# Optimization experiments

Measured on AMD Instinct MI355X. Metric: run time of the kernel, lower is better.

## Reference

```python
import jax, jax.numpy as jnp
import numpy as np

B, S, DIN, DOUT = 4, 4096, 2048, 8192


def setup_inputs() -> dict:
    key = jax.random.key(0)
    k1, k2 = jax.random.split(key)
    x = jax.random.normal(k1, (B, S, DIN), dtype=jnp.float32)
    # kaiming_normal_ (fan_in mode, leaky_relu a=sqrt(5) default -> gain based) approx via std = sqrt(2/fan_in)
    weight = jax.random.normal(k2, (DOUT, DIN), dtype=jnp.float32) * np.sqrt(2.0 / DIN)
    bias = jnp.zeros((DOUT,), dtype=jnp.float32)
    gamma = jnp.ones((DIN,), dtype=jnp.float32)
    return {"x": x, "weight": weight, "bias": bias, "gamma": gamma}


def reference(x, weight, bias, gamma):
    # RMSNorm in fp32 (torch nn.RMSNorm, eps=None -> finfo(fp32).eps)
    eps = jnp.asarray(np.finfo(np.float32).eps, dtype=jnp.float32)
    ms = jnp.mean(x * x, axis=-1, keepdims=True)  # [B,S,1]
    xn = x * jax.lax.rsqrt(ms + eps) * gamma      # [B,S,DIN]
    # Ternary quantize weights: threshold = mean(|w|), values in {-1,0,+1}; STE for grads
    thr = jnp.mean(jnp.abs(weight))
    w_t = jnp.sign(weight) * (jnp.abs(weight) > thr).astype(weight.dtype)
    w = weight + jax.lax.stop_gradient(w_t - weight)
    # Linear: out = xn @ w.T + bias
    out = jnp.einsum('bsi,oi->bso', xn, w) + bias
    return out
```

## Files before the change

kernel.cpp:

```cpp
#include <hip/hip_runtime.h>

typedef unsigned short u16;
typedef unsigned int   u32;
typedef unsigned char  u8;
typedef __attribute__((ext_vector_type(4))) int   i32x4;

constexpr int B_ = 4, S_ = 4096, DIN_ = 2048, DOUT_ = 8192;
constexpr int M_ = B_ * S_;
constexpr int N_ = DOUT_;
constexpr int K_ = DIN_;
constexpr size_t NW_ = (size_t)DOUT_ * DIN_;

#define GPTR(p) ((const __attribute__((address_space(1))) void*)(p))
#define LPTR(p) ((__attribute__((address_space(3))) void*)(p))

#define SB0()   __builtin_amdgcn_sched_barrier(0)
#define BAR()   asm volatile("s_barrier" ::: "memory")
#define LGKM0() asm volatile("s_waitcnt lgkmcnt(0)" ::: "memory")
#define VM4()   asm volatile("s_waitcnt vmcnt(4)" ::: "memory")
#define VM0()   asm volatile("s_waitcnt vmcnt(0)" ::: "memory")

__global__ __launch_bounds__(256)
void abssum_kernel(const float* __restrict__ w, double* __restrict__ partials)
{
    const int tid = threadIdx.x;
    const float* base = w + (size_t)blockIdx.x * 16384 + tid * 4;
    double s = 0.0;
#pragma unroll
    for (int i = 0; i < 16; ++i) {
        float4 v = *(const float4*)(base + i * 1024);
        s += (double)fabsf(v.x) + (double)fabsf(v.y)
           + (double)fabsf(v.z) + (double)fabsf(v.w);
    }
#pragma unroll
    for (int o = 32; o; o >>= 1) s += __shfl_xor(s, o, 64);
    __shared__ double red[4];
    if ((tid & 63) == 0) red[tid >> 6] = s;
    __syncthreads();
    if (tid == 0) partials[blockIdx.x] = (red[0] + red[1]) + (red[2] + red[3]);
}

__global__ __launch_bounds__(1024)
void finalize_thr(const double* __restrict__ partials, double* __restrict__ thr)
{
    __shared__ double red[1024];
    const int tid = threadIdx.x;
    red[tid] = partials[tid];
    __syncthreads();
    for (int s = 512; s > 0; s >>= 1) {
        if (tid < s) red[tid] += red[tid + s];
        __syncthreads();
    }
    if (tid == 0) *thr = red[0] * (1.0 / (double)NW_);
}

__device__ __forceinline__ int tern(float w, double thr) {
    return (fabs((double)w) > thr) ? (w > 0.0f ? 1 : -1) : 0;
}

__global__ __launch_bounds__(256)
void ternarize_kernel(const float* __restrict__ w, const double* __restrict__ thr_p,
                      signed char* __restrict__ wt)
{
    const double thr = *thr_p;
    const size_t i = ((size_t)blockIdx.x * 256 + threadIdx.x) * 4;
    float4 v = *(const float4*)(w + i);
    union { signed char c[4]; u32 u; } p;
    p.c[0] = (signed char)tern(v.x, thr);
    p.c[1] = (signed char)tern(v.y, thr);
    p.c[2] = (signed char)tern(v.z, thr);
    p.c[3] = (signed char)tern(v.w, thr);
    *(u32*)(wt + i) = p.u;
}

__global__ __launch_bounds__(256)
void rmsnorm_q_kernel(const float* __restrict__ x, const float* __restrict__ gamma,
                      signed char* __restrict__ xn, float* __restrict__ scale)
{
    const int row = blockIdx.x;
    const int tid = threadIdx.x;
    const float* xr = x + (size_t)row * K_;
    float4 a = *(const float4*)(xr + tid * 8);
    float4 b = *(const float4*)(xr + tid * 8 + 4);
    float s = a.x*a.x + a.y*a.y + a.z*a.z + a.w*a.w
            + b.x*b.x + b.y*b.y + b.z*b.z + b.w*b.w;
#pragma unroll
    for (int o = 32; o; o >>= 1) s += __shfl_xor(s, o, 64);
    __shared__ float redsum[4];
    __shared__ float redmax[4];
    if ((tid & 63) == 0) redsum[tid >> 6] = s;
    __syncthreads();
    const float tot = (redsum[0] + redsum[1]) + (redsum[2] + redsum[3]);
    const float r = rsqrtf(tot * (1.0f / (float)K_) + 1.1920928955078125e-07f);
    float4 g0 = *(const float4*)(gamma + tid * 8);
    float4 g1 = *(const float4*)(gamma + tid * 8 + 4);
    float v[8];
    v[0] = a.x * r * g0.x;  v[1] = a.y * r * g0.y;
    v[2] = a.z * r * g0.z;  v[3] = a.w * r * g0.w;
    v[4] = b.x * r * g1.x;  v[5] = b.y * r * g1.y;
    v[6] = b.z * r * g1.z;  v[7] = b.w * r * g1.w;
    float m = 0.0f;
#pragma unroll
    for (int j = 0; j < 8; ++j) m = fmaxf(m, fabsf(v[j]));
#pragma unroll
    for (int o = 32; o; o >>= 1) m = fmaxf(m, __shfl_xor(m, o, 64));
    if ((tid & 63) == 0) redmax[tid >> 6] = m;
    __syncthreads();
    const float rowmax = fmaxf(fmaxf(redmax[0], redmax[1]), fmaxf(redmax[2], redmax[3]));
    const float inv = rowmax > 0.0f ? 127.0f / rowmax : 0.0f;
    union { signed char c[8]; uint2 u; } p;
#pragma unroll
    for (int j = 0; j < 8; ++j) p.c[j] = (signed char)__float2int_rn(v[j] * inv);
    *(uint2*)(xn + (size_t)row * K_ + tid * 8) = p.u;
    if (tid == 0) scale[row] = rowmax * (1.0f / 127.0f);
}

__global__ __launch_bounds__(512, 2)
void gemm_bt_kernel(const u8* __restrict__ A, const u8* __restrict__ Bt,
                    const float* __restrict__ bias, const float* __restrict__ scale,
                    float* __restrict__ C)
{
    __shared__ alignas(16) u8 sm[131072];
    const char* smc = (const char*)sm;

    const int tid  = threadIdx.x;
    const int lane = tid & 63;
    const int wid  = tid >> 6;
    const int wm   = wid >> 2;
    const int wn   = wid & 3;
    const int hi   = lane >> 4;

    const int swz = (blockIdx.x & 7) * 256 + (blockIdx.x >> 3);
    const int gm0 = (swz >> 5) * 256;
    const int gn0 = (swz & 31) * 256;

    const int lr8   = lane >> 3;
    const int cswel = ((lane & 7) ^ lr8) * 16;
    const int rbase = wid * 8 + lr8;
    const u8* gAr  = A  + (size_t)(gm0 + rbase) * K_ + cswel;
    const u8* gBr  = Bt + (size_t)(gn0 + rbase) * K_ + cswel;
    const u8* gAr2 = gAr + 262144;
    const u8* gBr2 = gBr + 262144;

    auto STAGE = [&](const u8* g, int ldsb, int kt) {
        u8* d = sm + ldsb + wid * 1024 + lane * 16;
        const u8* s = g + kt;
        __builtin_amdgcn_global_load_lds(GPTR(s),             LPTR(d),        16, 0, 0);
        __builtin_amdgcn_global_load_lds(GPTR(s + 64 * 2048), LPTR(d + 8192), 16, 0, 0);
    };

    const int c0 = ((hi ^ (lane & 7)) << 4);
    const int rowbyteA = (wm * 128 + (lane & 15)) * 128;
    const int rowbyteB = (wn * 64  + (lane & 15)) * 128;

#define RA(bufr, m, kk) (*(const i32x4*)(smc + (bufr)*32768 + rowbyteA + (m)*2048 + (c0 ^ ((kk) << 6))))
#define RB(bufr, n, kk) (*(const i32x4*)(smc + 65536 + (bufr)*32768 + rowbyteB + (n)*2048 + (c0 ^ ((kk) << 6))))

    i32x4 acc[8][4] = {};
    i32x4 a0[4][2], a1[4][2], b0[2][2], b1[2][2];

#define MFMA_BLK(AF, BF, MO, NO)                                                   \
    do {                                                                           \
        _Pragma("unroll") for (int kk = 0; kk < 2; ++kk)                           \
        _Pragma("unroll") for (int m = 0; m < 4; ++m)                              \
        _Pragma("unroll") for (int n = 0; n < 2; ++n)                              \
            acc[m + MO][n + NO] = __builtin_amdgcn_mfma_i32_16x16x64_i8(           \
                AF[m][kk], BF[n][kk], acc[m + MO][n + NO], 0, 0, 0);               \
    } while (0)

#define READ_A0B0(bufr)                                                            \
    do {                                                                           \
        _Pragma("unroll") for (int m = 0; m < 4; ++m) {                            \
            a0[m][0] = RA(bufr, m, 0); a0[m][1] = RA(bufr, m, 1); }                \
        _Pragma("unroll") for (int n = 0; n < 2; ++n) {                            \
            b0[n][0] = RB(bufr, n, 0); b0[n][1] = RB(bufr, n, 1); }                \
    } while (0)
#define READ_A1(bufr)                                                              \
    do { _Pragma("unroll") for (int m = 0; m < 4; ++m) {                           \
            a1[m][0] = RA(bufr, m + 4, 0); a1[m][1] = RA(bufr, m + 4, 1); } } while (0)
#define READ_B1(bufr)                                                              \
    do { _Pragma("unroll") for (int n = 0; n < 2; ++n) {                           \
            b1[n][0] = RB(bufr, n + 2, 0); b1[n][1] = RB(bufr, n + 2, 1); } } while (0)

#define PRIO_MFMA(AF, BF, MO, NO)                                                  \
    do { __builtin_amdgcn_s_setprio(1); MFMA_BLK(AF, BF, MO, NO);                  \
         __builtin_amdgcn_s_setprio(0); } while (0)

    STAGE(gAr,  0,     0);
    STAGE(gAr2, 16384, 0);
    STAGE(gBr,  65536, 0);
    STAGE(gBr2, 81920, 0);
    STAGE(gAr,  32768, 128);
    STAGE(gAr2, 49152, 128);
    VM4(); SB0(); BAR();

    for (int i = 0; i < 8; ++i) {
        const int kt1  = i * 256 + 128;
        const int ktn0 = i * 256 + 256;
        const int ktn1 = i * 256 + 384;
        const bool f = (i < 7);

        READ_A0B0(0);
        STAGE(gBr, 98304, kt1);
        SB0(); BAR(); LGKM0(); SB0();
        PRIO_MFMA(a0, b0, 0, 0);
        SB0(); BAR();

        READ_A1(0);
        STAGE(gBr2, 114688, kt1);
        SB0(); BAR(); LGKM0(); SB0();
        PRIO_MFMA(a1, b0, 4, 0);
        SB0(); BAR();

        READ_B1(0);
        if (f) STAGE(gAr, 0, ktn0);
        SB0(); BAR(); LGKM0(); SB0();
        PRIO_MFMA(a0, b1, 0, 2);
        SB0(); BAR();

        if (f) STAGE(gAr2, 16384, ktn0);
        SB0(); BAR();
        PRIO_MFMA(a1, b1, 4, 2);
        SB0();
        if (f) { VM4(); } else { VM0(); }
        SB0(); BAR();

        READ_A0B0(1);
        if (f) STAGE(gBr, 65536, ktn0);
        SB0(); BAR(); LGKM0(); SB0();
        PRIO_MFMA(a0, b0, 0, 0);
        SB0(); BAR();

        READ_A1(1);
        if (f) STAGE(gBr2, 81920, ktn0);
        SB0(); BAR(); LGKM0(); SB0();
        PRIO_MFMA(a1, b0, 4, 0);
        SB0(); BAR();

        READ_B1(1);
        if (f) STAGE(gAr, 32768, ktn1);
        SB0(); BAR(); LGKM0(); SB0();
        PRIO_MFMA(a0, b1, 0, 2);
        SB0(); BAR();

        if (f) STAGE(gAr2, 49152, ktn1);
        SB0(); BAR();
        PRIO_MFMA(a1, b1, 4, 2);
        SB0();
        if (f) { VM4(); }
        SB0(); BAR();
    }

    const int orow0 = gm0 + wm * 128 + hi * 4;
    const int ocol0 = gn0 + wn * 64 + (lane & 15);
    float bv[4];
#pragma unroll
    for (int n = 0; n < 4; ++n) bv[n] = bias[ocol0 + n * 16];
#pragma unroll
    for (int m = 0; m < 8; ++m) {
#pragma unroll
        for (int ri = 0; ri < 4; ++ri) {
            const int row = orow0 + m * 16 + ri;
            const float sc = scale[row];
#pragma unroll
            for (int n = 0; n < 4; ++n) {
                C[(size_t)row * N_ + (ocol0 + n * 16)] = (float)acc[m][n][ri] * sc + bv[n];
            }
        }
    }
#undef RA
#undef RB
#undef MFMA_BLK
#undef READ_A0B0
#undef READ_A1
#undef READ_B1
#undef PRIO_MFMA
}

extern "C" void kernel_launch(void* const* d_in, const int* in_sizes, int n_in,
                              void* d_out, int out_size, void* d_ws, size_t ws_size,
                              hipStream_t stream)
{
    const float* x     = (const float*)d_in[0];
    const float* w     = (const float*)d_in[1];
    const float* bias  = (const float*)d_in[2];
    const float* gamma = (const float*)d_in[3];
    float* out = (float*)d_out;

    char* ws = (char*)d_ws;
    double*      thr      = (double*)(ws);
    double*      partials = (double*)(ws + 1024);
    signed char* wt       = (signed char*)(ws + 16384);
    signed char* xn       = (signed char*)(ws + 16384 + NW_);
    float*       scale    = (float*)(ws + 16384 + NW_ + (size_t)M_ * K_);

    abssum_kernel   <<<1024,  256,  0, stream>>>(w, partials);
    finalize_thr    <<<1,     1024, 0, stream>>>(partials, thr);
    ternarize_kernel<<<16384, 256,  0, stream>>>(w, thr, wt);
    rmsnorm_q_kernel<<<M_,    256,  0, stream>>>(x, gamma, xn, scale);
    gemm_bt_kernel  <<<(M_/256)*(N_/256), 512, 0, stream>>>((const u8*)xn, (const u8*)wt, bias, scale, out);
}
```

Before: 403.6 us.

## Shrink GEMM tile to 128x128 with 4 waves and fuse ternarize into rmsnorm

The int8 GEMM moves from 256x256 tiles with 512 threads and 128KB LDS to 128x128 tiles with 256 threads and 64KB LDS. This gives 4x more blocks, and the grid swizzle and staging are adjusted to match. Separately, the ternarize and rmsnorm-quantize kernels are merged into one launch whose extra blocks handle the weights, saving a launch. Smaller tiles lower per-block arithmetic intensity and increase global/L2 traffic, in exchange for more blocks and possibly better occupancy.

```diff
diff --git a/kernel.cpp b/kernel.cpp
--- a/kernel.cpp
+++ b/kernel.cpp
@@ -54,31 +54,30 @@
     if (tid == 0) *thr = red[0] * (1.0 / (double)NW_);
 }
 
-__device__ __forceinline__ int tern(float w, double thr) {
-    return (fabs((double)w) > thr) ? (w > 0.0f ? 1 : -1) : 0;
-}
-
 __global__ __launch_bounds__(256)
-void ternarize_kernel(const float* __restrict__ w, const double* __restrict__ thr_p,
-                      signed char* __restrict__ wt)
-{
-    const double thr = *thr_p;
-    const size_t i = ((size_t)blockIdx.x * 256 + threadIdx.x) * 4;
-    float4 v = *(const float4*)(w + i);
-    union { signed char c[4]; u32 u; } p;
-    p.c[0] = (signed char)tern(v.x, thr);
-    p.c[1] = (signed char)tern(v.y, thr);
-    p.c[2] = (signed char)tern(v.z, thr);
-    p.c[3] = (signed char)tern(v.w, thr);
-    *(u32*)(wt + i) = p.u;
-}
-
-__global__ __launch_bounds__(256)
-void rmsnorm_q_kernel(const float* __restrict__ x, const float* __restrict__ gamma,
-                      signed char* __restrict__ xn, float* __restrict__ scale)
-{
+void prep_kernel(const float* __restrict__ x, const float* __restrict__ gamma,
+                 const double* __restrict__ thr_p, const float* __restrict__ w,
+                 signed char* __restrict__ wt,
+                 signed char* __restrict__ xn, float* __restrict__ scale)
+{
+    __shared__ float redsum[4];
+    __shared__ float redmax[4];
+    const int tid = threadIdx.x;
+
+    if (blockIdx.x >= (unsigned)M_) {
+        const double thr = *thr_p;
+        const size_t i = ((size_t)(blockIdx.x - M_) * 256 + tid) * 4;
+        float4 v = *(const float4*)(w + i);
+        union { signed char c[4]; u32 u; } p;
+        p.c[0] = (signed char)((fabs((double)v.x) > thr) ? (v.x > 0.0f ? 1 : -1) : 0);
+        p.c[1] = (signed char)((fabs((double)v.y) > thr) ? (v.y > 0.0f ? 1 : -1) : 0);
+        p.c[2] = (signed char)((fabs((double)v.z) > thr) ? (v.z > 0.0f ? 1 : -1) : 0);
+        p.c[3] = (signed char)((fabs((double)v.w) > thr) ? (v.w > 0.0f ? 1 : -1) : 0);
+        *(u32*)(wt + i) = p.u;
+        return;
+    }
+
     const int row = blockIdx.x;
-    const int tid = threadIdx.x;
     const float* xr = x + (size_t)row * K_;
     float4 a = *(const float4*)(xr + tid * 8);
     float4 b = *(const float4*)(xr + tid * 8 + 4);
@@ -86,8 +85,6 @@
             + b.x*b.x + b.y*b.y + b.z*b.z + b.w*b.w;
 #pragma unroll
     for (int o = 32; o; o >>= 1) s += __shfl_xor(s, o, 64);
-    __shared__ float redsum[4];
-    __shared__ float redmax[4];
     if ((tid & 63) == 0) redsum[tid >> 6] = s;
     __syncthreads();
     const float tot = (redsum[0] + redsum[1]) + (redsum[2] + redsum[3]);
@@ -115,54 +112,52 @@
     if (tid == 0) scale[row] = rowmax * (1.0f / 127.0f);
 }
 
-__global__ __launch_bounds__(512, 2)
+__global__ __launch_bounds__(256, 2)
 void gemm_bt_kernel(const u8* __restrict__ A, const u8* __restrict__ Bt,
                     const float* __restrict__ bias, const float* __restrict__ scale,
                     float* __restrict__ C)
 {
-    __shared__ alignas(16) u8 sm[131072];
+    __shared__ alignas(16) u8 sm[65536];
     const char* smc = (const char*)sm;
 
     const int tid  = threadIdx.x;
     const int lane = tid & 63;
     const int wid  = tid >> 6;
-    const int wm   = wid >> 2;
-    const int wn   = wid & 3;
+    const int wm   = wid >> 1;
+    const int wn   = wid & 1;
     const int hi   = lane >> 4;
 
-    const int swz = (blockIdx.x & 7) * 256 + (blockIdx.x >> 3);
-    const int gm0 = (swz >> 5) * 256;
-    const int gn0 = (swz & 31) * 256;
-
-    const int lr8   = lane >> 3;
-    const int cswel = ((lane & 7) ^ lr8) * 16;
-    const int rbase = wid * 8 + lr8;
-    const u8* gAr  = A  + (size_t)(gm0 + rbase) * K_ + cswel;
-    const u8* gBr  = Bt + (size_t)(gn0 + rbase) * K_ + cswel;
-    const u8* gAr2 = gAr + 262144;
-    const u8* gBr2 = gBr + 262144;
-
-    auto STAGE = [&](const u8* g, int ldsb, int kt) {
-        u8* d = sm + ldsb + wid * 1024 + lane * 16;
-        const u8* s = g + kt;
-        __builtin_amdgcn_global_load_lds(GPTR(s),             LPTR(d),        16, 0, 0);
-        __builtin_amdgcn_global_load_lds(GPTR(s + 64 * 2048), LPTR(d + 8192), 16, 0, 0);
+    const int swz = (blockIdx.x & 7) * 1024 + (blockIdx.x >> 3);
+    const int gm0 = (swz >> 6) * 128;
+    const int gn0 = (swz & 63) * 128;
+
+    const int cswel = ((tid & 7) ^ ((tid >> 3) & 7)) * 16;
+    const u8* gA = A  + (size_t)(gm0 + (tid >> 3)) * K_ + cswel;
+    const u8* gB = Bt + (size_t)(gn0 + (tid >> 3)) * K_ + cswel;
+
+    auto STAGE2 = [&](const u8* g, int ldsb, int kt, int j) {
+        u8* d = sm + ldsb + j * 4096 + tid * 16;
+        const u8* s = g + (size_t)j * 32 * K_ + kt;
+        __builtin_amdgcn_global_load_lds(GPTR(s),                   LPTR(d),        16, 0, 0);
+        __builtin_amdgcn_global_load_lds(GPTR(s + (size_t)32 * K_), LPTR(d + 4096), 16, 0, 0);
     };
+#define ABUF(b) ((b) * 16384)
+#define BBUF(b) (32768 + (b) * 16384)
 
     const int c0 = ((hi ^ (lane & 7)) << 4);
-    const int rowbyteA = (wm * 128 + (lane & 15)) * 128;
-    const int rowbyteB = (wn * 64  + (lane & 15)) * 128;
-
-#define RA(bufr, m, kk) (*(const i32x4*)(smc + (bufr)*32768 + rowbyteA + (m)*2048 + (c0 ^ ((kk) << 6))))
-#define RB(bufr, n, kk) (*(const i32x4*)(smc + 65536 + (bufr)*32768 + rowbyteB + (n)*2048 + (c0 ^ ((kk) << 6))))
-
-    i32x4 acc[8][4] = {};
-    i32x4 a0[4][2], a1[4][2], b0[2][2], b1[2][2];
+    const int rowbyteA = (wm * 64 + (lane & 15)) * 128;
+    const int rowbyteB = (wn * 64 + (lane & 15)) * 128;
+
+#define RA(bufr, m, kk) (*(const i32x4*)(smc + (bufr)*16384 + rowbyteA + (m)*2048 + (c0 ^ ((kk) << 6))))
+#define RB(bufr, n, kk) (*(const i32x4*)(smc + 32768 + (bufr)*16384 + rowbyteB + (n)*2048 + (c0 ^ ((kk) << 6))))
+
+    i32x4 acc[4][4] = {};
+    i32x4 a0[2][2], a1[2][2], b0[2][2], b1[2][2];
 
 #define MFMA_BLK(AF, BF, MO, NO)                                                   \
     do {                                                                           \
         _Pragma("unroll") for (int kk = 0; kk < 2; ++kk)                           \
-        _Pragma("unroll") for (int m = 0; m < 4; ++m)                              \
+        _Pragma("unroll") for (int m = 0; m < 2; ++m)                              \
         _Pragma("unroll") for (int n = 0; n < 2; ++n)                              \
             acc[m + MO][n + NO] = __builtin_amdgcn_mfma_i32_16x16x64_i8(           \
                 AF[m][kk], BF[n][kk], acc[m + MO][n + NO], 0, 0, 0);               \
@@ -170,14 +165,14 @@
 
 #define READ_A0B0(bufr)                                                            \
     do {                                                                           \
-        _Pragma("unroll") for (int m = 0; m < 4; ++m) {                            \
+        _Pragma("unroll") for (int m = 0; m < 2; ++m) {                            \
             a0[m][0] = RA(bufr, m, 0); a0[m][1] = RA(bufr, m, 1); }                \
         _Pragma("unroll") for (int n = 0; n < 2; ++n) {                            \
             b0[n][0] = RB(bufr, n, 0); b0[n][1] = RB(bufr, n, 1); }                \
     } while (0)
 #define READ_A1(bufr)                                                              \
-    do { _Pragma("unroll") for (int m = 0; m < 4; ++m) {                           \
-            a1[m][0] = RA(bufr, m + 4, 0); a1[m][1] = RA(bufr, m + 4, 1); } } while (0)
+    do { _Pragma("unroll") for (int m = 0; m < 2; ++m) {                           \
+            a1[m][0] = RA(bufr, m + 2, 0); a1[m][1] = RA(bufr, m + 2, 1); } } while (0)
 #define READ_B1(bufr)                                                              \
     do { _Pragma("unroll") for (int n = 0; n < 2; ++n) {                           \
             b1[n][0] = RB(bufr, n + 2, 0); b1[n][1] = RB(bufr, n + 2, 1); } } while (0)
@@ -186,12 +181,9 @@
     do { __builtin_amdgcn_s_setprio(1); MFMA_BLK(AF, BF, MO, NO);                  \
          __builtin_amdgcn_s_setprio(0); } while (0)
 
-    STAGE(gAr,  0,     0);
-    STAGE(gAr2, 16384, 0);
-    STAGE(gBr,  65536, 0);
-    STAGE(gBr2, 81920, 0);
-    STAGE(gAr,  32768, 128);
-    STAGE(gAr2, 49152, 128);
+    STAGE2(gA, ABUF(0), 0, 0);   STAGE2(gA, ABUF(0), 0, 2);
+    STAGE2(gB, BBUF(0), 0, 0);   STAGE2(gB, BBUF(0), 0, 2);
+    STAGE2(gA, ABUF(1), 128, 0); STAGE2(gA, ABUF(1), 128, 2);
     VM4(); SB0(); BAR();
 
     for (int i = 0; i < 8; ++i) {
@@ -201,63 +193,63 @@
         const bool f = (i < 7);
 
         READ_A0B0(0);
-        STAGE(gBr, 98304, kt1);
+        STAGE2(gB, BBUF(1), kt1, 0);
         SB0(); BAR(); LGKM0(); SB0();
         PRIO_MFMA(a0, b0, 0, 0);
         SB0(); BAR();
 
         READ_A1(0);
-        STAGE(gBr2, 114688, kt1);
-        SB0(); BAR(); LGKM0(); SB0();
-        PRIO_MFMA(a1, b0, 4, 0);
+        STAGE2(gB, BBUF(1), kt1, 2);
+        SB0(); BAR(); LGKM0(); SB0();
+        PRIO_MFMA(a1, b0, 2, 0);
         SB0(); BAR();
 
         READ_B1(0);
-        if (f) STAGE(gAr, 0, ktn0);
+        if (f) STAGE2(gA, ABUF(0), ktn0, 0);
         SB0(); BAR(); LGKM0(); SB0();
         PRIO_MFMA(a0, b1, 0, 2);
         SB0(); BAR();
 
-        if (f) STAGE(gAr2, 16384, ktn0);
-        SB0(); BAR();
-        PRIO_MFMA(a1, b1, 4, 2);
+        if (f) STAGE2(gA, ABUF(0), ktn0, 2);
+        SB0(); BAR();
+        PRIO_MFMA(a1, b1, 2, 2);
         SB0();
         if (f) { VM4(); } else { VM0(); }
         SB0(); BAR();
 
         READ_A0B0(1);
-        if (f) STAGE(gBr, 65536, ktn0);
+        if (f) STAGE2(gB, BBUF(0), ktn0, 0);
         SB0(); BAR(); LGKM0(); SB0();
         PRIO_MFMA(a0, b0, 0, 0);
         SB0(); BAR();
 
         READ_A1(1);
-        if (f) STAGE(gBr2, 81920, ktn0);
-        SB0(); BAR(); LGKM0(); SB0();
-        PRIO_MFMA(a1, b0, 4, 0);
+        if (f) STAGE2(gB, BBUF(0), ktn0, 2);
+        SB0(); BAR(); LGKM0(); SB0();
+        PRIO_MFMA(a1, b0, 2, 0);
         SB0(); BAR();
 
         READ_B1(1);
-        if (f) STAGE(gAr, 32768, ktn1);
+        if (f) STAGE2(gA, ABUF(1), ktn1, 0);
         SB0(); BAR(); LGKM0(); SB0();
         PRIO_MFMA(a0, b1, 0, 2);
         SB0(); BAR();
 
-        if (f) STAGE(gAr2, 49152, ktn1);
-        SB0(); BAR();
-        PRIO_MFMA(a1, b1, 4, 2);
+        if (f) STAGE2(gA, ABUF(1), ktn1, 2);
+        SB0(); BAR();
+        PRIO_MFMA(a1, b1, 2, 2);
         SB0();
         if (f) { VM4(); }
         SB0(); BAR();
     }
 
-    const int orow0 = gm0 + wm * 128 + hi * 4;
+    const int orow0 = gm0 + wm * 64 + hi * 4;
     const int ocol0 = gn0 + wn * 64 + (lane & 15);
     float bv[4];
 #pragma unroll
     for (int n = 0; n < 4; ++n) bv[n] = bias[ocol0 + n * 16];
 #pragma unroll
-    for (int m = 0; m < 8; ++m) {
+    for (int m = 0; m < 4; ++m) {
 #pragma unroll
         for (int ri = 0; ri < 4; ++ri) {
             const int row = orow0 + m * 16 + ri;
@@ -275,6 +267,8 @@
 #undef READ_A1
 #undef READ_B1
 #undef PRIO_MFMA
+#undef ABUF
+#undef BBUF
 }
 
 extern "C" void kernel_launch(void* const* d_in, const int* in_sizes, int n_in,
@@ -294,9 +288,8 @@
     signed char* xn       = (signed char*)(ws + 16384 + NW_);
     float*       scale    = (float*)(ws + 16384 + NW_ + (size_t)M_ * K_);
 
-    abssum_kernel   <<<1024,  256,  0, stream>>>(w, partials);
-    finalize_thr    <<<1,     1024, 0, stream>>>(partials, thr);
-    ternarize_kernel<<<16384, 256,  0, stream>>>(w, thr, wt);
-    rmsnorm_q_kernel<<<M_,    256,  0, stream>>>(x, gamma, xn, scale);
-    gemm_bt_kernel  <<<(M_/256)*(N_/256), 512, 0, stream>>>((const u8*)xn, (const u8*)wt, bias, scale, out);
-}
+    abssum_kernel <<<1024,  256,  0, stream>>>(w, partials);
+    finalize_thr  <<<1,     1024, 0, stream>>>(partials, thr);
+    prep_kernel   <<<M_ + 16384, 256, 0, stream>>>(x, gamma, thr, w, wt, xn, scale);
+    gemm_bt_kernel<<<(M_/128)*(N_/128), 256, 0, stream>>>((const u8*)xn, (const u8*)wt, bias, scale, out);
+}
```

Measured after the change: 484.1 us. +20.0%, slower.
